# Kernel optimization log

Hardware: AMD Instinct MI355X
Metric: run time of the kernel (lower is better)

Reference implementation:

```python
import jax, jax.numpy as jnp
import numpy as np

DIM = 1024
HEADS = 16
HEAD_DIM = DIM // HEADS


def setup_inputs() -> dict:
    key = jax.random.key(0)
    k1, k2, k3, k4 = jax.random.split(key, 4)
    x = jax.random.normal(k1, (4, 4096, DIM), dtype=jnp.float32)
    # nn.Linear(dim, 3*dim, bias=False): weight [3*dim, dim]
    w_qkv = jax.random.normal(k2, (3 * DIM, DIM), dtype=jnp.float32) * (DIM ** -0.5)
    # nn.Linear(dim, dim): weight [dim, dim], bias [dim]
    w_proj = jax.random.normal(k3, (DIM, DIM), dtype=jnp.float32) * (DIM ** -0.5)
    b_proj = jax.random.normal(k4, (DIM,), dtype=jnp.float32) * 0.01
    return {"x": x, "w_qkv": w_qkv, "w_proj": w_proj, "b_proj": b_proj}


def reference(x, w_qkv, w_proj, b_proj):
    B, N, C = x.shape
    H, D = HEADS, HEAD_DIM
    qkv = x @ w_qkv.T                                    # [B, N, 3C]
    qkv = qkv.reshape(B, N, 3, H, D).transpose(2, 0, 3, 1, 4)  # [3, B, H, N, D]
    q, k, v = qkv[0], qkv[1], qkv[2]
    # elu(x) + 1 feature map (positive kernel)
    q = jax.nn.elu(q) + 1.0
    k = jax.nn.elu(k) + 1.0
    kv = jnp.einsum('bhnd,bhne->bhde', k, v)             # [B, H, D, D]
    num = jnp.einsum('bhnd,bhde->bhne', q, kv)           # [B, H, N, D]
    k_sum = k.sum(axis=-2)                               # [B, H, D]
    qk = jnp.einsum('bhnd,bhd->bhn', q, k_sum)[..., None]  # [B, H, N, 1]
    out = num / (qk + 1e-8)                              # [B, H, N, D]
    out = out.transpose(0, 2, 1, 3).reshape(B, N, C)
    return out @ w_proj.T + b_proj
```

## Files before the change

kernel.cpp:

```cpp
#include <hip/hip_runtime.h>
#include <hip/hip_bf16.h>
#include <stdint.h>

typedef __hip_bfloat16 bf16;
typedef __attribute__((ext_vector_type(4))) float f32x4;
typedef __attribute__((ext_vector_type(8))) short short8;

#define SEQ   4096
#define CDIM  1024

__device__ __forceinline__ void async_load16(const void* g, void* l) {
  auto gp = reinterpret_cast<const __attribute__((address_space(1))) uint32_t*>(
      reinterpret_cast<uintptr_t>(g));
  auto lp = reinterpret_cast<__attribute__((address_space(3))) uint32_t*>(
      static_cast<uint32_t>(reinterpret_cast<uintptr_t>(l)));
  __builtin_amdgcn_global_load_lds(gp, lp, 16, 0, 0);
}

__global__ __launch_bounds__(256) void convert3_kernel(const float* __restrict__ x,
                                                       const float* __restrict__ wq,
                                                       const float* __restrict__ wp,
                                                       bf16* __restrict__ xb,
                                                       bf16* __restrict__ wqb,
                                                       bf16* __restrict__ wpb) {
  int i = blockIdx.x * 256 + threadIdx.x;
  const float* src;
  bf16* dst;
  int off;
  if (i < 4194304)      { src = x;  dst = xb;  off = i; }
  else if (i < 4980736) { src = wq; dst = wqb; off = i - 4194304; }
  else                  { src = wp; dst = wpb; off = i - 4980736; }
  float4 f = ((const float4*)src)[off];
  union { bf16 b[4]; ushort4 u; } c;
  c.b[0] = __float2bfloat16(f.x);
  c.b[1] = __float2bfloat16(f.y);
  c.b[2] = __float2bfloat16(f.z);
  c.b[3] = __float2bfloat16(f.w);
  ((ushort4*)dst)[off] = c.u;
}

#define BARR()  __builtin_amdgcn_s_barrier()
#define LGKM0() asm volatile("s_waitcnt lgkmcnt(0)" ::: "memory")
#define VMW6()  asm volatile("s_waitcnt vmcnt(6)" ::: "memory")
#define VMW0()  asm volatile("s_waitcnt vmcnt(0)" ::: "memory")
#define SP(x)   __builtin_amdgcn_s_setprio(x)

#define STA(buf, kc, h)                                                        \
  {                                                                            \
    const int ra_ = (h) * 64 + w * 8;                                          \
    async_load16(Ag + (size_t)(ra_ + lr8) * K + (kc) + cs, (buf) + ra_ * 64);  \
    async_load16(Ag + (size_t)(ra_ + 128 + lr8) * K + (kc) + cs,               \
                 (buf) + (ra_ + 128) * 64);                                    \
  }
#define STB(buf, kc, h)                                                        \
  {                                                                            \
    const int rb_ = (w & 3) * 8 + (w >> 2) * 64 + (h) * 32;                    \
    async_load16(Bg + (size_t)(rb_ + lr8) * K + (kc) + cs, (buf) + rb_ * 64);  \
    async_load16(Bg + (size_t)(rb_ + 128 + lr8) * K + (kc) + cs,               \
                 (buf) + (rb_ + 128) * 64);                                    \
  }

#define RD_A(buf, h)                                                           \
  {                                                                            \
    _Pragma("unroll") for (int mi = 0; mi < 4; ++mi) {                         \
      const unsigned short* p_ = (buf) + (arow0 + (h) * 64 + mi * 16) * 64;    \
      af[mi][0] = *(const short8*)(p_ + ((lq * 8) ^ sw));                      \
      af[mi][1] = *(const short8*)(p_ + ((32 + lq * 8) ^ sw));                 \
    }                                                                          \
  }
#define RD_B(buf, h)                                                           \
  {                                                                            \
    _Pragma("unroll") for (int ni = 0; ni < 2; ++ni) {                         \
      const unsigned short* p_ = (buf) + (brow0 + (h) * 32 + ni * 16) * 64;    \
      bfr[ni][0] = *(const short8*)(p_ + ((lq * 8) ^ sw));                     \
      bfr[ni][1] = *(const short8*)(p_ + ((32 + lq * 8) ^ sw));                \
    }                                                                          \
  }

#define MMA(MQ, NQ)                                                            \
  {                                                                            \
    _Pragma("unroll") for (int ks = 0; ks < 2; ++ks)                           \
      _Pragma("unroll") for (int mi = 0; mi < 4; ++mi)                         \
        _Pragma("unroll") for (int ni = 0; ni < 2; ++ni)                       \
          acc[(MQ) * 4 + mi][(NQ) * 2 + ni] =                                  \
              __builtin_amdgcn_mfma_f32_16x16x32_bf16(                         \
                  af[mi][ks], bfr[ni][ks], acc[(MQ) * 4 + mi][(NQ) * 2 + ni],  \
                  0, 0, 0);                                                    \
  }

#define FULL_ITER(kc)                                                          \
  RD_A(A0, 0); RD_B(B0, 0); STB(B1, (kc) + 64, 0);                             \
  BARR(); LGKM0(); SP(1); MMA(0, 0); SP(0); BARR();                            \
  RD_B(B0, 1); STA(A0, (kc) + 128, 0);                                         \
  BARR(); LGKM0(); SP(1); MMA(0, 1); SP(0); BARR();                            \
  RD_A(A0, 1); STB(B0, (kc) + 128, 1);                                         \
  BARR(); LGKM0(); SP(1); MMA(1, 1); SP(0); BARR();                            \
  RD_B(B0, 0); STA(A0, (kc) + 128, 1); VMW6();                                 \
  BARR(); LGKM0(); SP(1); MMA(1, 0); SP(0); BARR();                            \
  RD_A(A1, 0); RD_B(B1, 0); STB(B0, (kc) + 128, 0);                            \
  BARR(); LGKM0(); SP(1); MMA(0, 0); SP(0); BARR();                            \
  RD_B(B1, 1); STA(A1, (kc) + 192, 0);                                         \
  BARR(); LGKM0(); SP(1); MMA(0, 1); SP(0); BARR();                            \
  RD_A(A1, 1); STB(B1, (kc) + 192, 1);                                         \
  BARR(); LGKM0(); SP(1); MMA(1, 1); SP(0); BARR();                            \
  RD_B(B1, 0); STA(A1, (kc) + 192, 1); VMW6();                                 \
  BARR(); LGKM0(); SP(1); MMA(1, 0); SP(0); BARR();

#define FINAL_ITER(kc)                                                         \
  RD_A(A0, 0); RD_B(B0, 0); STB(B1, (kc) + 64, 0);                             \
  BARR(); LGKM0(); SP(1); MMA(0, 0); SP(0); BARR();                            \
  RD_B(B0, 1);                                                                 \
  BARR(); LGKM0(); SP(1); MMA(0, 1); SP(0); BARR();                            \
  RD_A(A0, 1);                                                                 \
  BARR(); LGKM0(); SP(1); MMA(1, 1); SP(0); BARR();                            \
  RD_B(B0, 0); VMW0();                                                         \
  BARR(); LGKM0(); SP(1); MMA(1, 0); SP(0); BARR();                            \
  RD_A(A1, 0); RD_B(B1, 0);                                                    \
  BARR(); LGKM0(); SP(1); MMA(0, 0); SP(0); BARR();                            \
  RD_B(B1, 1);                                                                 \
  BARR(); LGKM0(); SP(1); MMA(0, 1); SP(0); BARR();                            \
  RD_A(A1, 1);                                                                 \
  BARR(); LGKM0(); SP(1); MMA(1, 1); SP(0); BARR();                            \
  RD_B(B1, 0);                                                                 \
  LGKM0(); SP(1); MMA(1, 0); SP(0);

template <int EPI>
__global__ __launch_bounds__(512, 2) void gemm256(const bf16* __restrict__ X,
                                                  const bf16* __restrict__ W,
                                                  const float* __restrict__ bias,
                                                  bf16* __restrict__ Qo,
                                                  bf16* __restrict__ Ko,
                                                  bf16* __restrict__ Vo,
                                                  float* __restrict__ Out,
                                                  const int K) {
  __shared__ __attribute__((aligned(16))) unsigned short lds[4][256 * 64];
  unsigned short* const A0 = lds[0];
  unsigned short* const B0 = lds[1];
  unsigned short* const A1 = lds[2];
  unsigned short* const B1 = lds[3];

  const int tid  = threadIdx.x;
  const int w    = tid >> 6, lane = tid & 63;
  const int wm   = w >> 2,   wn   = w & 3;
  const int lr   = lane & 15, lq  = lane >> 4;
  const int bm   = blockIdx.y, bn = blockIdx.x;
  const int sw   = (lr & 7) << 3;
  const int cs   = (((lane & 7) ^ (lane >> 3)) << 3);
  const int lr8  = lane >> 3;

  const bool swapped = (EPI == 0) && (bn < 4);
  const bf16* Xg = X + (size_t)(bm * 256) * K;
  const bf16* Wg = W + (size_t)(bn * 256) * K;
  const bf16* Ag = swapped ? Wg : Xg;
  const bf16* Bg = swapped ? Xg : Wg;

  const int arow0 = wm * 128 + lr;
  const int brow0 = wn * 64 + lr;

  short8 af[4][2], bfr[2][2];
  f32x4 acc[8][4] = {};

  STA(A0, 0, 0);
  STB(B0, 0, 0);
  STB(B0, 0, 1);
  STA(A0, 0, 1);
  STA(A1, 64, 0);
  STB(B1, 64, 1);
  STA(A1, 64, 1);
  VMW6();
  BARR();

#pragma unroll 1
  for (int kc = 0; kc < K - 128; kc += 128) {
    FULL_ITER(kc);
  }
  FINAL_ITER(K - 128);

  if constexpr (EPI == 0) {
    if (swapped) {
#pragma unroll
      for (int mt = 0; mt < 8; ++mt) {
        const int j0 = bn * 256 + wm * 128 + mt * 16 + lq * 4;
        const int h  = j0 >> 6, d0 = j0 & 63;
#pragma unroll
        for (int nt = 0; nt < 4; ++nt) {
          const int t = bm * 256 + wn * 64 + nt * 16 + lr;
          const int b = t >> 12, n = t & 4095;
          union { bf16 v[4]; ushort4 u; } pk;
#pragma unroll
          for (int r = 0; r < 4; ++r) {
            float v = acc[mt][nt][r];
            v = (v > 0.0f) ? (v + 1.0f) : __expf(v);
            pk.v[r] = __float2bfloat16(v);
          }
          *(ushort4*)(Qo + (((size_t)((b * 16 + h) * SEQ + n)) << 6) + d0) = pk.u;
        }
      }
    } else {
#pragma unroll
      for (int nt = 0; nt < 4; ++nt) {
        const int j   = bn * 256 + wn * 64 + nt * 16 + lr;
        const int sel = j >> 10;
        const int h   = (j >> 6) & 15;
        const int d   = j & 63;
        bf16* dst = (sel == 1) ? Ko : Vo;
#pragma unroll
        for (int mt = 0; mt < 8; ++mt) {
          const int t0 = bm * 256 + wm * 128 + mt * 16 + lq * 4;
          const int b = t0 >> 12, n0 = t0 & 4095;
          union { bf16 v[4]; ushort4 u; } pk;
#pragma unroll
          for (int r = 0; r < 4; ++r) {
            float v = acc[mt][nt][r];
            if (sel == 1) v = (v > 0.0f) ? (v + 1.0f) : __expf(v);
            pk.v[r] = __float2bfloat16(v);
          }
          *(ushort4*)(dst + ((size_t)((b * 16 + h) * 64 + d)) * SEQ + n0) = pk.u;
        }
      }
    }
  } else {
#pragma unroll
    for (int mt = 0; mt < 8; ++mt) {
#pragma unroll
      for (int r = 0; r < 4; ++r) {
        const int t = bm * 256 + wm * 128 + mt * 16 + lq * 4 + r;
        float* op = Out + (size_t)t * CDIM + bn * 256 + wn * 64 + lr;
#pragma unroll
        for (int nt = 0; nt < 4; ++nt)
          op[nt * 16] = acc[mt][nt][r] + bias[bn * 256 + wn * 64 + nt * 16 + lr];
      }
    }
  }
}

__global__ __launch_bounds__(256) void kv_mfma(const bf16* __restrict__ KT,
                                               const bf16* __restrict__ VT,
                                               float* __restrict__ KVp,
                                               float* __restrict__ KSp) {
  __shared__ bf16 kt[64 * 64];
  __shared__ bf16 vt[64 * 64];
  const int tid = threadIdx.x;
  const int w = tid >> 6, lane = tid & 63;
  const int wm = w >> 1, wn = w & 1;
  const int lr = lane & 15, lq = lane >> 4;
  const int swz = (lr & 7) * 8;
  const int csz = (((lane & 7) ^ (lane >> 3)) * 8);
  const int sp = blockIdx.x, bh = blockIdx.y;
  const bf16* kg0 = KT + (size_t)bh * 64 * SEQ + sp * 512;
  const bf16* vg0 = VT + (size_t)bh * 64 * SEQ + sp * 512;

  f32x4 acc[2][2] = {};
  f32x4 kacc0 = {}, kacc1 = {};
  short8 ones;
#pragma unroll
  for (int j = 0; j < 8; ++j) ((unsigned short*)&ones)[j] = 0x3F80;

  for (int nc = 0; nc < 8; ++nc) {
    __syncthreads();
#pragma unroll
    for (int i = 0; i < 2; ++i) {
      const int row = w * 16 + i * 8 + (lane >> 3);
      async_load16(kg0 + (size_t)row * SEQ + nc * 64 + csz, kt + (w * 16 + i * 8) * 64);
      async_load16(vg0 + (size_t)row * SEQ + nc * 64 + csz, vt + (w * 16 + i * 8) * 64);
    }
    __syncthreads();

#pragma unroll
    for (int ks = 0; ks < 2; ++ks) {
      short8 a0 = *(const short8*)&kt[(wm * 32 +      lr) * 64 + ((ks * 32 + lq * 8) ^ swz)];
      short8 a1 = *(const short8*)&kt[(wm * 32 + 16 + lr) * 64 + ((ks * 32 + lq * 8) ^ swz)];
      short8 b0 = *(const short8*)&vt[(wn * 32 +      lr) * 64 + ((ks * 32 + lq * 8) ^ swz)];
      short8 b1 = *(const short8*)&vt[(wn * 32 + 16 + lr) * 64 + ((ks * 32 + lq * 8) ^ swz)];
      acc[0][0] = __builtin_amdgcn_mfma_f32_16x16x32_bf16(a0, b0, acc[0][0], 0, 0, 0);
      acc[0][1] = __builtin_amdgcn_mfma_f32_16x16x32_bf16(a0, b1, acc[0][1], 0, 0, 0);
      acc[1][0] = __builtin_amdgcn_mfma_f32_16x16x32_bf16(a1, b0, acc[1][0], 0, 0, 0);
      acc[1][1] = __builtin_amdgcn_mfma_f32_16x16x32_bf16(a1, b1, acc[1][1], 0, 0, 0);
      kacc0 = __builtin_amdgcn_mfma_f32_16x16x32_bf16(a0, ones, kacc0, 0, 0, 0);
      kacc1 = __builtin_amdgcn_mfma_f32_16x16x32_bf16(a1, ones, kacc1, 0, 0, 0);
    }
  }

  float* outp = KVp + ((size_t)(sp * 64 + bh)) * 4096;
#pragma unroll
  for (int mt = 0; mt < 2; ++mt)
#pragma unroll
    for (int nt = 0; nt < 2; ++nt) {
      const int e  = wn * 32 + nt * 16 + lr;
      const int d0 = wm * 32 + mt * 16 + lq * 4;
      *(float4*)&outp[e * 64 + d0] = *(float4*)&acc[mt][nt];
    }
  if (wn == 0 && lr == 0) {
    float* ksp = KSp + (size_t)(sp * 64 + bh) * 64 + wm * 32;
#pragma unroll
    for (int r = 0; r < 4; ++r) {
      ksp[lq * 4 + r]      = kacc0[r];
      ksp[16 + lq * 4 + r] = kacc1[r];
    }
  }
}

__global__ __launch_bounds__(256) void kv_reduce(const float* __restrict__ KVp,
                                                 const float* __restrict__ KSp,
                                                 bf16* __restrict__ KVT,
                                                 float* __restrict__ KS) {
  const int bh = blockIdx.x, t = threadIdx.x;
#pragma unroll 4
  for (int i = 0; i < 16; ++i) {
    const int idx = i * 256 + t;
    float s = 0.0f;
#pragma unroll
    for (int sp = 0; sp < 8; ++sp) s += KVp[((size_t)(sp * 64 + bh)) * 4096 + idx];
    const bf16 hi = __float2bfloat16(s);
    const float lo = s - __bfloat162float(hi);
    const int e = idx >> 6, d = idx & 63;
    KVT[(size_t)bh * 8192 + e * 128 + d]      = hi;
    KVT[(size_t)bh * 8192 + e * 128 + 64 + d] = __float2bfloat16(lo);
  }
  if (t < 64) {
    float s = 0.0f;
#pragma unroll
    for (int sp = 0; sp < 8; ++sp) s += KSp[(sp * 64 + bh) * 64 + t];
    KS[bh * 64 + t] = s;
  }
}

__global__ __launch_bounds__(256) void num_mfma(const bf16* __restrict__ Qb,
                                                const bf16* __restrict__ KVT,
                                                const float* __restrict__ KS,
                                                bf16* __restrict__ Attn) {
  __shared__ bf16 qs[128 * 64];
  __shared__ bf16 kvs[64 * 128];
  __shared__ bf16 Cs[128 * 72];
  __shared__ float ksl[64];
  __shared__ float dred[256];
  __shared__ float den[128];
  const int tid = threadIdx.x;
  const int w = tid >> 6, lane = tid & 63;
  const int wm = w >> 1, wn = w & 1;
  const int lr = lane & 15, lq = lane >> 4;
  const int swz = (lr & 7) * 8;
  const int bh = blockIdx.y, n00 = blockIdx.x * 128;
  const int b = bh >> 4, h = bh & 15;

  const bf16* qg  = Qb  + ((size_t)bh * SEQ + n00) * 64;
  const bf16* kvg = KVT + (size_t)bh * 8192;
  const int qcs = (((lane & 7) ^ (lane >> 3)) * 8);
#pragma unroll
  for (int i = 0; i < 4; ++i) {
    const int row = w * 32 + i * 8 + (lane >> 3);
    async_load16(qg + (size_t)row * 64 + qcs, qs + (w * 32 + i * 8) * 64);
  }
#pragma unroll
  for (int i = 0; i < 4; ++i) {
    const int row = w * 16 + i * 4 + (lane >> 4);
    const int scol = (((lane & 15) * 8) ^ ((row & 7) * 8));
    async_load16(kvg + (size_t)row * 128 + scol, kvs + (w * 16 + i * 4) * 128);
  }
  if (tid < 64) ksl[tid] = KS[bh * 64 + tid];
  __syncthreads();

  {
    const int n = tid >> 1, half = tid & 1;
    const int nsw = (n & 7) * 8;
    float s = 0.0f;
#pragma unroll
    for (int v8 = 0; v8 < 4; ++v8) {
      short8 qq = *(const short8*)&qs[n * 64 + ((half * 32 + v8 * 8) ^ nsw)];
#pragma unroll
      for (int j = 0; j < 8; ++j)
        s += __bfloat162float(((const bf16*)&qq)[j]) * ksl[half * 32 + v8 * 8 + j];
    }
    dred[tid] = s;
  }

  short8 afr[4][2], bfr2[2][4];
#pragma unroll
  for (int mt = 0; mt < 4; ++mt)
#pragma unroll
    for (int kh = 0; kh < 2; ++kh)
      afr[mt][kh] = *(const short8*)&qs[(wm * 64 + mt * 16 + lr) * 64 + ((kh * 32 + lq * 8) ^ swz)];
#pragma unroll
  for (int nt = 0; nt < 2; ++nt)
#pragma unroll
    for (int ks = 0; ks < 4; ++ks)
      bfr2[nt][ks] = *(const short8*)&kvs[(wn * 32 + nt * 16 + lr) * 128 + ((ks * 32 + lq * 8) ^ swz)];

  f32x4 acc[4][2] = {};
#pragma unroll
  for (int ks = 0; ks < 4; ++ks)
#pragma unroll
    for (int mt = 0; mt < 4; ++mt)
#pragma unroll
      for (int nt = 0; nt < 2; ++nt)
        acc[mt][nt] = __builtin_amdgcn_mfma_f32_16x16x32_bf16(afr[mt][ks & 1], bfr2[nt][ks],
                                                              acc[mt][nt], 0, 0, 0);
  __syncthreads();
  if (tid < 128) den[tid] = dred[tid * 2] + dred[tid * 2 + 1] + 1e-8f;
  __syncthreads();

#pragma unroll
  for (int mt = 0; mt < 4; ++mt) {
#pragma unroll
    for (int r = 0; r < 4; ++r) {
      const int nl = wm * 64 + mt * 16 + lq * 4 + r;
      const float inv = 1.0f / den[nl];
#pragma unroll
      for (int nt = 0; nt < 2; ++nt) {
        const int e = wn * 32 + nt * 16 + lr;
        Cs[nl * 72 + e] = __float2bfloat16(acc[mt][nt][r] * inv);
      }
    }
  }
  __syncthreads();
#pragma unroll
  for (int it = 0; it < 4; ++it) {
    const int nl = it * 32 + (tid >> 3);
    const int ch = tid & 7;
    short8 val = *(const short8*)&Cs[nl * 72 + ch * 8];
    *(short8*)(Attn + ((size_t)(b * SEQ + n00 + nl)) * CDIM + h * 64 + ch * 8) = val;
  }
}

extern "C" void kernel_launch(void* const* d_in, const int* in_sizes, int n_in,
                              void* d_out, int out_size, void* d_ws, size_t ws_size,
                              hipStream_t stream) {
  const float* x      = (const float*)d_in[0];
  const float* w_qkv  = (const float*)d_in[1];
  const float* w_proj = (const float*)d_in[2];
  const float* b_proj = (const float*)d_in[3];
  float* out = (float*)d_out;
  char* ws = (char*)d_ws;

  bf16*  xb     = (bf16*)(ws + 0);
  bf16*  wqkvb  = (bf16*)(ws + 33554432);
  bf16*  wprojb = (bf16*)(ws + 39845888);
  bf16*  qb     = (bf16*)(ws + 41943040);
  bf16*  ktb    = (bf16*)(ws + 75497472);
  bf16*  vtb    = (bf16*)(ws + 109051904);
  float* kvp    = (float*)(ws + 0);
  float* ksp    = (float*)(ws + 8388608);
  bf16*  kvt    = (bf16*)(ws + 142606336);
  float* ksum   = (float*)(ws + 143654912);
  bf16*  attn   = (bf16*)(ws + 0);

  convert3_kernel<<<20480, 256, 0, stream>>>(x, w_qkv, w_proj, xb, wqkvb, wprojb);

  gemm256<0><<<dim3(12, 64), 512, 0, stream>>>(xb, wqkvb, nullptr, qb, ktb, vtb, nullptr, 1024);
  kv_mfma<<<dim3(8, 64), 256, 0, stream>>>(ktb, vtb, kvp, ksp);
  kv_reduce<<<64, 256, 0, stream>>>(kvp, ksp, kvt, ksum);
  num_mfma<<<dim3(32, 64), 256, 0, stream>>>(qb, kvt, ksum, attn);
  gemm256<1><<<dim3(4, 64), 512, 0, stream>>>(attn, wprojb, b_proj, nullptr, nullptr, nullptr, out, 1024);
}
```

Before: 316.7 us.

## Keep B fragments in registers, remap GEMM tiles across XCDs, widen kv_reduce grid

```diff
diff --git a/kernel.cpp b/kernel.cpp
--- a/kernel.cpp
+++ b/kernel.cpp
@@ -72,8 +72,8 @@
   {                                                                            \
     _Pragma("unroll") for (int ni = 0; ni < 2; ++ni) {                         \
       const unsigned short* p_ = (buf) + (brow0 + (h) * 32 + ni * 16) * 64;    \
-      bfr[ni][0] = *(const short8*)(p_ + ((lq * 8) ^ sw));                     \
-      bfr[ni][1] = *(const short8*)(p_ + ((32 + lq * 8) ^ sw));                \
+      bfr[h][ni][0] = *(const short8*)(p_ + ((lq * 8) ^ sw));                  \
+      bfr[h][ni][1] = *(const short8*)(p_ + ((32 + lq * 8) ^ sw));             \
     }                                                                          \
   }
 
@@ -84,8 +84,8 @@
         _Pragma("unroll") for (int ni = 0; ni < 2; ++ni)                       \
           acc[(MQ) * 4 + mi][(NQ) * 2 + ni] =                                  \
               __builtin_amdgcn_mfma_f32_16x16x32_bf16(                         \
-                  af[mi][ks], bfr[ni][ks], acc[(MQ) * 4 + mi][(NQ) * 2 + ni],  \
-                  0, 0, 0);                                                    \
+                  af[mi][ks], bfr[NQ][ni][ks],                                 \
+                  acc[(MQ) * 4 + mi][(NQ) * 2 + ni], 0, 0, 0);                 \
   }
 
 #define FULL_ITER(kc)                                                          \
@@ -95,16 +95,16 @@
   BARR(); LGKM0(); SP(1); MMA(0, 1); SP(0); BARR();                            \
   RD_A(A0, 1); STB(B0, (kc) + 128, 1);                                         \
   BARR(); LGKM0(); SP(1); MMA(1, 1); SP(0); BARR();                            \
-  RD_B(B0, 0); STA(A0, (kc) + 128, 1); VMW6();                                 \
-  BARR(); LGKM0(); SP(1); MMA(1, 0); SP(0); BARR();                            \
+  STA(A0, (kc) + 128, 1); VMW6();                                              \
+  BARR(); SP(1); MMA(1, 0); SP(0); BARR();                                     \
   RD_A(A1, 0); RD_B(B1, 0); STB(B0, (kc) + 128, 0);                            \
   BARR(); LGKM0(); SP(1); MMA(0, 0); SP(0); BARR();                            \
   RD_B(B1, 1); STA(A1, (kc) + 192, 0);                                         \
   BARR(); LGKM0(); SP(1); MMA(0, 1); SP(0); BARR();                            \
   RD_A(A1, 1); STB(B1, (kc) + 192, 1);                                         \
   BARR(); LGKM0(); SP(1); MMA(1, 1); SP(0); BARR();                            \
-  RD_B(B1, 0); STA(A1, (kc) + 192, 1); VMW6();                                 \
-  BARR(); LGKM0(); SP(1); MMA(1, 0); SP(0); BARR();
+  STA(A1, (kc) + 192, 1); VMW6();                                              \
+  BARR(); SP(1); MMA(1, 0); SP(0); BARR();
 
 #define FINAL_ITER(kc)                                                         \
   RD_A(A0, 0); RD_B(B0, 0); STB(B1, (kc) + 64, 0);                             \
@@ -113,16 +113,15 @@
   BARR(); LGKM0(); SP(1); MMA(0, 1); SP(0); BARR();                            \
   RD_A(A0, 1);                                                                 \
   BARR(); LGKM0(); SP(1); MMA(1, 1); SP(0); BARR();                            \
-  RD_B(B0, 0); VMW0();                                                         \
-  BARR(); LGKM0(); SP(1); MMA(1, 0); SP(0); BARR();                            \
+  VMW0();                                                                      \
+  BARR(); SP(1); MMA(1, 0); SP(0); BARR();                                     \
   RD_A(A1, 0); RD_B(B1, 0);                                                    \
   BARR(); LGKM0(); SP(1); MMA(0, 0); SP(0); BARR();                            \
   RD_B(B1, 1);                                                                 \
   BARR(); LGKM0(); SP(1); MMA(0, 1); SP(0); BARR();                            \
   RD_A(A1, 1);                                                                 \
   BARR(); LGKM0(); SP(1); MMA(1, 1); SP(0); BARR();                            \
-  RD_B(B1, 0);                                                                 \
-  LGKM0(); SP(1); MMA(1, 0); SP(0);
+  SP(1); MMA(1, 0); SP(0);
 
 template <int EPI>
 __global__ __launch_bounds__(512, 2) void gemm256(const bf16* __restrict__ X,
@@ -143,7 +142,14 @@
   const int w    = tid >> 6, lane = tid & 63;
   const int wm   = w >> 2,   wn   = w & 3;
   const int lr   = lane & 15, lq  = lane >> 4;
-  const int bm   = blockIdx.y, bn = blockIdx.x;
+
+  const int GX   = (int)gridDim.x;
+  const int nwg  = GX * (int)gridDim.y;
+  const int lin  = (int)blockIdx.y * GX + (int)blockIdx.x;
+  const int tile = (lin & 7) * (nwg >> 3) + (lin >> 3);
+  const int bn   = tile % GX;
+  const int bm   = tile / GX;
+
   const int sw   = (lr & 7) << 3;
   const int cs   = (((lane & 7) ^ (lane >> 3)) << 3);
   const int lr8  = lane >> 3;
@@ -157,7 +163,7 @@
   const int arow0 = wm * 128 + lr;
   const int brow0 = wn * 64 + lr;
 
-  short8 af[4][2], bfr[2][2];
+  short8 af[4][2], bfr[2][2][2];
   f32x4 acc[8][4] = {};
 
   STA(A0, 0, 0);
@@ -304,10 +310,10 @@
                                                  const float* __restrict__ KSp,
                                                  bf16* __restrict__ KVT,
                                                  float* __restrict__ KS) {
-  const int bh = blockIdx.x, t = threadIdx.x;
-#pragma unroll 4
-  for (int i = 0; i < 16; ++i) {
-    const int idx = i * 256 + t;
+  const int bh = blockIdx.x >> 2, q = blockIdx.x & 3, t = threadIdx.x;
+#pragma unroll
+  for (int i = 0; i < 4; ++i) {
+    const int idx = (q * 4 + i) * 256 + t;
     float s = 0.0f;
 #pragma unroll
     for (int sp = 0; sp < 8; ++sp) s += KVp[((size_t)(sp * 64 + bh)) * 4096 + idx];
@@ -317,7 +323,7 @@
     KVT[(size_t)bh * 8192 + e * 128 + d]      = hi;
     KVT[(size_t)bh * 8192 + e * 128 + 64 + d] = __float2bfloat16(lo);
   }
-  if (t < 64) {
+  if (q == 0 && t < 64) {
     float s = 0.0f;
 #pragma unroll
     for (int sp = 0; sp < 8; ++sp) s += KSp[(sp * 64 + bh) * 64 + t];
@@ -448,7 +454,7 @@
 
   gemm256<0><<<dim3(12, 64), 512, 0, stream>>>(xb, wqkvb, nullptr, qb, ktb, vtb, nullptr, 1024);
   kv_mfma<<<dim3(8, 64), 256, 0, stream>>>(ktb, vtb, kvp, ksp);
-  kv_reduce<<<64, 256, 0, stream>>>(kvp, ksp, kvt, ksum);
+  kv_reduce<<<256, 256, 0, stream>>>(kvp, ksp, kvt, ksum);
   num_mfma<<<dim3(32, 64), 256, 0, stream>>>(qb, kvt, ksum, attn);
   gemm256<1><<<dim3(4, 64), 512, 0, stream>>>(attn, wprojb, b_proj, nullptr, nullptr, nullptr, out, 1024);
 }
```

Measured after the change: 304.9 us. 1.04x faster.
